# Performance work log

Measured on AMD Instinct MI355X. Metric: run time of the kernel, lower is better.

The kernel has to match this reference:

```python
import jax, jax.numpy as jnp
import numpy as np

EMBED = 1024
HEADS = 16
HEAD_DIM = EMBED // HEADS
MLP_HIDDEN = 4096


def _layernorm(x, g, b, eps=1e-5):
    mu = jnp.mean(x, axis=-1, keepdims=True)
    var = jnp.mean(jnp.square(x - mu), axis=-1, keepdims=True)
    return (x - mu) * jax.lax.rsqrt(var + eps) * g + b


def setup_inputs() -> dict:
    key = jax.random.key(0)
    ks = jax.random.split(key, 8)
    s = 0.02
    return {
        "x": jax.random.normal(ks[0], (8, 1024, EMBED), dtype=jnp.float32),
        "qkv_w": jax.random.normal(ks[1], (EMBED, 3 * EMBED), dtype=jnp.float32) * s,
        "qkv_b": jnp.zeros((3 * EMBED,), jnp.float32),
        "proj_w": jax.random.normal(ks[2], (EMBED, EMBED), dtype=jnp.float32) * s,
        "proj_b": jnp.zeros((EMBED,), jnp.float32),
        "fc1_w": jax.random.normal(ks[3], (EMBED, MLP_HIDDEN), dtype=jnp.float32) * s,
        "fc1_b": jnp.zeros((MLP_HIDDEN,), jnp.float32),
        "fc2_w": jax.random.normal(ks[4], (MLP_HIDDEN, EMBED), dtype=jnp.float32) * s,
        "fc2_b": jnp.zeros((EMBED,), jnp.float32),
        "ln1_g": jnp.ones((EMBED,), jnp.float32),
        "ln1_b": jnp.zeros((EMBED,), jnp.float32),
        "ln2_g": jnp.ones((EMBED,), jnp.float32),
        "ln2_b": jnp.zeros((EMBED,), jnp.float32),
    }


def reference(x, qkv_w, qkv_b, proj_w, proj_b, fc1_w, fc1_b, fc2_w, fc2_b,
              ln1_g, ln1_b, ln2_g, ln2_b):
    B, N, C = x.shape
    scale = HEAD_DIM ** -0.5

    # --- MHSA on pre-norm input ---
    h = _layernorm(x, ln1_g, ln1_b)
    qkv = h @ qkv_w + qkv_b                      # [B,N,3C]
    qkv = qkv.reshape(B, N, 3, HEADS, HEAD_DIM)
    q, k, v = (qkv[:, :, i].transpose(0, 2, 1, 3) for i in range(3))  # [B,H,N,d]
    attn = jnp.einsum('bhqd,bhkd->bhqk', q, k) * scale
    attn = jax.nn.softmax(attn, axis=-1)
    o = jnp.einsum('bhqk,bhkd->bhqd', attn, v)   # [B,H,N,d]
    o = o.transpose(0, 2, 1, 3).reshape(B, N, C)
    x = x + (o @ proj_w + proj_b)

    # --- MLP ---
    h2 = _layernorm(x, ln2_g, ln2_b)
    h2 = jax.nn.gelu(h2 @ fc1_w + fc1_b, approximate=False)
    x = x + (h2 @ fc2_w + fc2_b)
    return x
```

## Files before the change

kernel.cpp:

```cpp
#include <hip/hip_runtime.h>
#include <hip/hip_bf16.h>

typedef __bf16 bf16x8 __attribute__((ext_vector_type(8)));
typedef float  f32x4  __attribute__((ext_vector_type(4)));
typedef unsigned short u16;

static __device__ __forceinline__ u16 f2bf(float f) {
  union { float f; unsigned u; } v; v.f = f;
  unsigned r = v.u + 0x7fffu + ((v.u >> 16) & 1u);
  return (u16)(r >> 16);
}

static __device__ __forceinline__ void gld16(const void* g, void* l) {
  __builtin_amdgcn_global_load_lds(
      (const __attribute__((address_space(1))) unsigned int*)g,
      (__attribute__((address_space(3))) unsigned int*)l, 16, 0, 0);
}

#define SBAR() do { __builtin_amdgcn_sched_barrier(0); \
                    __builtin_amdgcn_s_barrier(); \
                    __builtin_amdgcn_sched_barrier(0); } while (0)

__global__ __launch_bounds__(256) void prep_k(
    const float* __restrict__ qkv_w, const float* __restrict__ proj_w,
    const float* __restrict__ fc1_w, const float* __restrict__ fc2_w,
    u16* __restrict__ wqkvT, u16* __restrict__ wprojT,
    u16* __restrict__ wfc1T, u16* __restrict__ wfc2T,
    const float* __restrict__ x, const float* __restrict__ g,
    const float* __restrict__ b, u16* __restrict__ hbuf) {
  const int bid = blockIdx.x;
  const int t = threadIdx.x;
  if (bid < 12288) {
    __shared__ float tile[32][33];
    const float* W; u16* Wt; int K, N, nx, i;
    if (bid < 3072)      { W = qkv_w;  Wt = wqkvT;  K = 1024; N = 3072; nx = 96;  i = bid; }
    else if (bid < 4096) { W = proj_w; Wt = wprojT; K = 1024; N = 1024; nx = 32;  i = bid - 3072; }
    else if (bid < 8192) { W = fc1_w;  Wt = wfc1T;  K = 1024; N = 4096; nx = 128; i = bid - 4096; }
    else                 { W = fc2_w;  Wt = wfc2T;  K = 4096; N = 1024; nx = 32;  i = bid - 8192; }
    const int n0 = (i % nx) * 32, k0 = (i / nx) * 32;
    const int r = t >> 3, c4 = (t & 7) * 4;
    const float4 v = *(const float4*)(W + (size_t)(k0 + r) * N + n0 + c4);
    tile[r][c4 + 0] = v.x; tile[r][c4 + 1] = v.y;
    tile[r][c4 + 2] = v.z; tile[r][c4 + 3] = v.w;
    __syncthreads();
    const int n = t >> 3, k4 = (t & 7) * 4;
    uint2 pk;
    pk.x = f2bf(tile[k4 + 0][n]) | ((unsigned)f2bf(tile[k4 + 1][n]) << 16);
    pk.y = f2bf(tile[k4 + 2][n]) | ((unsigned)f2bf(tile[k4 + 3][n]) << 16);
    *(uint2*)(Wt + (size_t)(n0 + n) * K + k0 + k4) = pk;
  } else {
    __shared__ float red[2][4];
    const size_t row = bid - 12288;
    const float4 v = *(const float4*)(x + row * 1024 + t * 4);
    float s = v.x + v.y + v.z + v.w;
    float ss = v.x * v.x + v.y * v.y + v.z * v.z + v.w * v.w;
    #pragma unroll
    for (int m = 1; m <= 32; m <<= 1) { s += __shfl_xor(s, m); ss += __shfl_xor(ss, m); }
    if ((t & 63) == 0) { red[0][t >> 6] = s; red[1][t >> 6] = ss; }
    __syncthreads();
    s  = red[0][0] + red[0][1] + red[0][2] + red[0][3];
    ss = red[1][0] + red[1][1] + red[1][2] + red[1][3];
    const float mu = s * (1.f / 1024.f);
    const float var = ss * (1.f / 1024.f) - mu * mu;
    const float rs = rsqrtf(var + 1e-5f);
    const float4 gv = *(const float4*)(g + t * 4);
    const float4 bv = *(const float4*)(b + t * 4);
    uint2 pk;
    pk.x = f2bf((v.x - mu) * rs * gv.x + bv.x) |
           ((unsigned)f2bf((v.y - mu) * rs * gv.y + bv.y) << 16);
    pk.y = f2bf((v.z - mu) * rs * gv.z + bv.z) |
           ((unsigned)f2bf((v.w - mu) * rs * gv.w + bv.w) << 16);
    *(uint2*)(hbuf + row * 1024 + t * 4) = pk;
  }
}

__global__ __launch_bounds__(256) void ln_cast_k(
    const float* __restrict__ x, const float* __restrict__ g,
    const float* __restrict__ b, u16* __restrict__ out) {
  __shared__ float red[2][4];
  const int t = threadIdx.x;
  const size_t row = blockIdx.x;
  const float4 v = *(const float4*)(x + row * 1024 + t * 4);
  float s = v.x + v.y + v.z + v.w;
  float ss = v.x * v.x + v.y * v.y + v.z * v.z + v.w * v.w;
  #pragma unroll
  for (int m = 1; m <= 32; m <<= 1) { s += __shfl_xor(s, m); ss += __shfl_xor(ss, m); }
  if ((t & 63) == 0) { red[0][t >> 6] = s; red[1][t >> 6] = ss; }
  __syncthreads();
  s  = red[0][0] + red[0][1] + red[0][2] + red[0][3];
  ss = red[1][0] + red[1][1] + red[1][2] + red[1][3];
  const float mu = s * (1.f / 1024.f);
  const float var = ss * (1.f / 1024.f) - mu * mu;
  const float rs = rsqrtf(var + 1e-5f);
  const float4 gv = *(const float4*)(g + t * 4);
  const float4 bv = *(const float4*)(b + t * 4);
  uint2 pk;
  pk.x = f2bf((v.x - mu) * rs * gv.x + bv.x) |
         ((unsigned)f2bf((v.y - mu) * rs * gv.y + bv.y) << 16);
  pk.y = f2bf((v.z - mu) * rs * gv.z + bv.z) |
         ((unsigned)f2bf((v.w - mu) * rs * gv.w + bv.w) << 16);
  *(uint2*)(out + row * 1024 + t * 4) = pk;
}

template <int EPI>
__global__ __launch_bounds__(512, 2) void gemm_k(
    const u16* __restrict__ A, const u16* __restrict__ Bt,
    const float* __restrict__ bias, u16* __restrict__ Cb, float* __restrict__ Cf,
    const float* __restrict__ R, u16* __restrict__ vT, int M, int N, int K) {
  __shared__ u16 SH[49152];
  const int t = threadIdx.x;
  const int nt = N >> 7;
  const int q = gridDim.x >> 3;
  const int swz = (blockIdx.x & 7) * q + (blockIdx.x >> 3);
  const int tn = swz % nt, tm = swz / nt;
  const int lo = t & 15, hi = (t >> 4) & 3, wid = t >> 6;
  const int wm = wid >> 1, wn = wid & 1;
  const int NT = K >> 6;

  const int srow = t >> 3;
  const int sc = (t & 7) ^ (srow & 7);
  const u16* gA = A  + (size_t)(tm * 256) * K;
  const u16* gB = Bt + (size_t)(tn * 128) * K;
  auto stA = [&](int dd, int c, int T) {
    gld16(gA + (size_t)(c * 64 + srow) * K + (size_t)T * 64 + sc * 8,
          &SH[dd * 16384 + c * 4096 + t * 8]);
  };
  auto stB = [&](int dd, int c, int T) {
    gld16(gB + (size_t)(c * 64 + srow) * K + (size_t)T * 64 + sc * 8,
          &SH[32768 + dd * 8192 + c * 4096 + t * 8]);
  };

  const int xr = lo & 7;
  const int rowA = wm * 64 + lo;
  const int rowB = wn * 64 + lo;
#define RD_A(d, m, kk) (*(const bf16x8*)&SH[(d)*16384 + (rowA + (m)*16)*64 + ((((kk)<<2)+hi)^xr)*8])
#define RD_B(d, n, kk) (*(const bf16x8*)&SH[32768 + (d)*8192 + (rowB + (n)*16)*64 + ((((kk)<<2)+hi)^xr)*8])
#define MF(a, b, c) __builtin_amdgcn_mfma_f32_16x16x32_bf16(a, b, c, 0, 0, 0)

  f32x4 acc[4][4];
  #pragma unroll
  for (int i = 0; i < 4; ++i)
    #pragma unroll
    for (int j = 0; j < 4; ++j) acc[i][j] = (f32x4){0.f, 0.f, 0.f, 0.f};

#define PH8(d, M0, STAGES, WAITS) do { \
    bf16x8 a0 = RD_A(d, M0, 0), a1 = RD_A(d, M0, 1); \
    STAGES; SBAR(); __builtin_amdgcn_s_setprio(1); \
    acc[M0][0]=MF(a0,b00,acc[M0][0]); acc[M0][1]=MF(a0,b10,acc[M0][1]); \
    acc[M0][2]=MF(a0,b20,acc[M0][2]); acc[M0][3]=MF(a0,b30,acc[M0][3]); \
    acc[M0][0]=MF(a1,b01,acc[M0][0]); acc[M0][1]=MF(a1,b11,acc[M0][1]); \
    acc[M0][2]=MF(a1,b21,acc[M0][2]); acc[M0][3]=MF(a1,b31,acc[M0][3]); \
    __builtin_amdgcn_s_setprio(0); WAITS; SBAR(); } while (0)

  stA(0, 0, 0); stA(0, 1, 0); stA(0, 2, 0); stA(0, 3, 0);
  stB(0, 0, 0); stB(0, 1, 0);
  stB(1, 0, 1); stB(1, 1, 1);
  asm volatile("s_waitcnt vmcnt(2)" ::: "memory");
  SBAR();

  for (int T = 0; T < NT; ++T) {
    const int d = T & 1, dn = d ^ 1;
    bf16x8 b00 = RD_B(d,0,0), b01 = RD_B(d,0,1), b10 = RD_B(d,1,0), b11 = RD_B(d,1,1);
    bf16x8 b20 = RD_B(d,2,0), b21 = RD_B(d,2,1), b30 = RD_B(d,3,0), b31 = RD_B(d,3,1);
    PH8(d, 0, { if (T + 1 < NT) { stA(dn, 0, T + 1); stA(dn, 1, T + 1);
                                  stA(dn, 2, T + 1); stA(dn, 3, T + 1); } }, );
    PH8(d, 1, { if (T + 2 < NT) { stB(d, 0, T + 2); stB(d, 1, T + 2); } }, );
    PH8(d, 2, , );
    PH8(d, 3, ,
        { if (T < NT - 2)       { asm volatile("s_waitcnt vmcnt(2)" ::: "memory"); }
          else if (T == NT - 2) { asm volatile("s_waitcnt vmcnt(0)" ::: "memory"); } });
  }

  if constexpr (EPI == 2) {
    #pragma unroll
    for (int ni = 0; ni < 4; ++ni) {
      const int col = tn * 128 + wn * 64 + ni * 16 + lo;
      const float bv = bias[col];
      #pragma unroll
      for (int mi = 0; mi < 4; ++mi) {
        const int row0 = tm * 256 + wm * 64 + mi * 16 + hi * 4;
        #pragma unroll
        for (int r = 0; r < 4; ++r) {
          const size_t idx = (size_t)(row0 + r) * N + col;
          Cf[idx] = acc[mi][ni][r] + bv + R[idx];
        }
      }
    }
  } else {
    #pragma unroll
    for (int ni = 0; ni < 4; ++ni) {
      const int colL = wn * 64 + ni * 16 + lo;
      const float bv = bias[tn * 128 + colL];
      #pragma unroll
      for (int mi = 0; mi < 4; ++mi) {
        const int rowL = wm * 64 + mi * 16 + hi * 4;
        #pragma unroll
        for (int r = 0; r < 4; ++r) {
          float val = acc[mi][ni][r] + bv;
          if (EPI == 1) {
            const float u = 0.79788456f * val * (1.f + 0.044715f * val * val);
            const float e = __expf(fminf(2.f * u, 80.f));
            val = val * (e / (e + 1.f));
          }
          SH[(rowL + r) * 128 + colL] = f2bf(val);
        }
      }
    }
    __syncthreads();
    {
      const int base = t * 16;
      #pragma unroll
      for (int p = 0; p < 8; ++p) {
        const int o = base + p * 8192;
        const int row = o >> 8;
        const int cb = (o & 255) >> 1;
        const uint4 v4 = *(const uint4*)&SH[o >> 1];
        *(uint4*)(Cb + (size_t)(tm * 256 + row) * N + tn * 128 + cb) = v4;
      }
    }
    if constexpr (EPI == 3) {
      if (tn >= 16) {
        const int c = t & 127;
        const int rg = t >> 7;
        const int gcol = tn * 128 + c;
        const int hh = (gcol - 2048) >> 6, dd = gcol & 63;
        const int bb = tm >> 2, nb = (tm & 3) * 256;
        u16* dst = vT + ((size_t)((bb * 16 + hh) * 64 + dd) << 10) + nb + rg * 64;
        #pragma unroll
        for (int i = 0; i < 8; ++i) {
          const int r0 = rg * 64 + i * 8;
          u16 tv[8];
          #pragma unroll
          for (int j = 0; j < 8; ++j) tv[j] = SH[(r0 + j) * 128 + c];
          uint4 pk;
          pk.x = tv[0] | ((unsigned)tv[1] << 16);
          pk.y = tv[2] | ((unsigned)tv[3] << 16);
          pk.z = tv[4] | ((unsigned)tv[5] << 16);
          pk.w = tv[6] | ((unsigned)tv[7] << 16);
          *(uint4*)(dst + i * 8) = pk;
        }
      }
    }
  }
#undef RD_A
#undef RD_B
#undef MF
#undef PH8
}

__global__ __launch_bounds__(256, 2) void attn_k(
    const u16* __restrict__ qkv, const u16* __restrict__ vT, u16* __restrict__ o) {
  __shared__ u16 lK[64 * 64];
  __shared__ u16 lV[64 * 64];
  __shared__ u16 lP[64 * 72];
  const int t = threadIdx.x;
  const int lo = t & 15, hi = (t >> 4) & 3, w = t >> 6;
  const int swz = (blockIdx.x & 7) * 256 + (blockIdx.x >> 3);
  const int qt = swz & 15, bh = swz >> 4;
  const int b = bh >> 4, h = bh & 15;
  const int q0 = qt * 64;
  const u16* Qb = qkv + (size_t)b * 1024 * 3072 + h * 64;
  const u16* Kb = Qb + 1024;
  const u16* Vt = vT + (size_t)bh * 64 * 1024;

  bf16x8 qf[2];
  {
    const size_t q = q0 + w * 16 + lo;
    qf[0] = *(const bf16x8*)(Qb + q * 3072 + hi * 8);
    qf[1] = *(const bf16x8*)(Qb + q * 3072 + 32 + hi * 8);
  }
  f32x4 oacc[4];
  #pragma unroll
  for (int i = 0; i < 4; ++i) oacc[i] = (f32x4){0.f, 0.f, 0.f, 0.f};
  float m = -1e30f, lsum = 0.f;
  const int srow = t >> 3;
  const int sc = (t & 7) ^ (srow & 7);
  const int xr = lo & 7;
  const float SC = 0.125f * 1.44269504f;

  for (int kv0 = 0; kv0 < 1024; kv0 += 64) {
    __syncthreads();
    #pragma unroll
    for (int j = 0; j < 2; ++j) {
      const int r64 = j * 32 + srow;
      gld16(Kb + (size_t)(kv0 + r64) * 3072 + sc * 8, &lK[(j * 256 + t) * 8]);
      gld16(Vt + (size_t)r64 * 1024 + kv0 + sc * 8, &lV[(j * 256 + t) * 8]);
    }
    __syncthreads();

    f32x4 s[4];
    #pragma unroll
    for (int i = 0; i < 4; ++i) s[i] = (f32x4){0.f, 0.f, 0.f, 0.f};
    #pragma unroll
    for (int kk = 0; kk < 2; ++kk) {
      #pragma unroll
      for (int mi = 0; mi < 4; ++mi) {
        const bf16x8 kf = *(const bf16x8*)&lK[(mi * 16 + lo) * 64 + (((kk << 2) + hi) ^ xr) * 8];
        s[mi] = __builtin_amdgcn_mfma_f32_16x16x32_bf16(kf, qf[kk], s[mi], 0, 0, 0);
      }
    }
    float sv[16];
    float tmax = -1e30f;
    #pragma unroll
    for (int mi = 0; mi < 4; ++mi)
      #pragma unroll
      for (int r = 0; r < 4; ++r) {
        const float xx = s[mi][r] * SC;
        sv[mi * 4 + r] = xx;
        tmax = fmaxf(tmax, xx);
      }
    tmax = fmaxf(tmax, __shfl_xor(tmax, 16));
    tmax = fmaxf(tmax, __shfl_xor(tmax, 32));
    if (__any(tmax > m + 11.5f)) {
      const float mnew = fmaxf(m, tmax);
      const float alpha = exp2f(m - mnew);
      m = mnew;
      lsum *= alpha;
      float ar[4];
      #pragma unroll
      for (int r = 0; r < 4; ++r) ar[r] = __shfl(alpha, hi * 4 + r);
      #pragma unroll
      for (int ni = 0; ni < 4; ++ni)
        #pragma unroll
        for (int r = 0; r < 4; ++r) oacc[ni][r] *= ar[r];
    }
    float p[16], ts = 0.f;
    #pragma unroll
    for (int i = 0; i < 16; ++i) { p[i] = exp2f(sv[i] - m); ts += p[i]; }
    ts += __shfl_xor(ts, 16);
    ts += __shfl_xor(ts, 32);
    lsum += ts;
    #pragma unroll
    for (int mi = 0; mi < 4; ++mi) {
      uint2 pk;
      pk.x = f2bf(p[mi * 4 + 0]) | ((unsigned)f2bf(p[mi * 4 + 1]) << 16);
      pk.y = f2bf(p[mi * 4 + 2]) | ((unsigned)f2bf(p[mi * 4 + 3]) << 16);
      *(uint2*)&lP[(w * 16 + lo) * 72 + mi * 16 + hi * 4] = pk;
    }
    asm volatile("s_waitcnt lgkmcnt(0)" ::: "memory");
    #pragma unroll
    for (int kk = 0; kk < 2; ++kk) {
      const bf16x8 pf = *(const bf16x8*)&lP[(w * 16 + lo) * 72 + kk * 32 + hi * 8];
      #pragma unroll
      for (int ni = 0; ni < 4; ++ni) {
        const bf16x8 vf = *(const bf16x8*)&lV[(ni * 16 + lo) * 64 + (((kk << 2) + hi) ^ xr) * 8];
        oacc[ni] = __builtin_amdgcn_mfma_f32_16x16x32_bf16(pf, vf, oacc[ni], 0, 0, 0);
      }
    }
  }
  float lr[4];
  #pragma unroll
  for (int r = 0; r < 4; ++r) lr[r] = 1.f / __shfl(lsum, hi * 4 + r);
  #pragma unroll
  for (int ni = 0; ni < 4; ++ni) {
    const int d = ni * 16 + lo;
    #pragma unroll
    for (int r = 0; r < 4; ++r) {
      const int n = q0 + w * 16 + hi * 4 + r;
      o[((size_t)(b * 1024 + n) * 16 + h) * 64 + d] = f2bf(oacc[ni][r] * lr[r]);
    }
  }
}

extern "C" void kernel_launch(void* const* d_in, const int* in_sizes, int n_in,
                              void* d_out, int out_size, void* d_ws, size_t ws_size,
                              hipStream_t stream) {
  const float* x      = (const float*)d_in[0];
  const float* qkv_w  = (const float*)d_in[1];
  const float* qkv_b  = (const float*)d_in[2];
  const float* proj_w = (const float*)d_in[3];
  const float* proj_b = (const float*)d_in[4];
  const float* fc1_w  = (const float*)d_in[5];
  const float* fc1_b  = (const float*)d_in[6];
  const float* fc2_w  = (const float*)d_in[7];
  const float* fc2_b  = (const float*)d_in[8];
  const float* ln1_g  = (const float*)d_in[9];
  const float* ln1_b  = (const float*)d_in[10];
  const float* ln2_g  = (const float*)d_in[11];
  const float* ln2_b  = (const float*)d_in[12];
  float* out = (float*)d_out;
  char* ws = (char*)d_ws;
  u16* wqkvT = (u16*)(ws);
  u16* wprojT = (u16*)(ws + 6291456);
  u16* wfc1T = (u16*)(ws + 8388608);
  u16* wfc2T = (u16*)(ws + 16777216);
  u16* hbuf  = (u16*)(ws + 25165824);
  u16* qkvo  = (u16*)(ws + 41943040);
  u16* vT    = (u16*)(ws + 92274688);
  u16* fc1o  = qkvo;

  prep_k<<<20480, 256, 0, stream>>>(qkv_w, proj_w, fc1_w, fc2_w,
                                    wqkvT, wprojT, wfc1T, wfc2T,
                                    x, ln1_g, ln1_b, hbuf);
  gemm_k<3><<<768, 512, 0, stream>>>(hbuf, wqkvT, qkv_b, qkvo, nullptr, nullptr, vT, 8192, 3072, 1024);
  attn_k<<<2048, 256, 0, stream>>>(qkvo, vT, hbuf);
  gemm_k<2><<<256, 512, 0, stream>>>(hbuf, wprojT, proj_b, nullptr, out, x, nullptr, 8192, 1024, 1024);
  ln_cast_k<<<8192, 256, 0, stream>>>(out, ln2_g, ln2_b, hbuf);
  gemm_k<1><<<1024, 512, 0, stream>>>(hbuf, wfc1T, fc1_b, fc1o, nullptr, nullptr, nullptr, 8192, 4096, 1024);
  gemm_k<2><<<256, 512, 0, stream>>>(fc1o, wfc2T, fc2_b, nullptr, out, out, nullptr, 8192, 1024, 4096);
}
```

Before: 399.1 us.

## Replace pipelined 256x128 GEMM with simple single-buffered 128x128 kernel

Swaps the double-buffered, barrier-scheduled 512-thread GEMM with 256x128 tiles for a plain 256-thread kernel that uses 128x128 tiles and a single LDS buffer. Each K step loads A and B, syncs, runs the MFMAs and syncs again. This shrinks LDS use and doubles the grid size, which may raise occupancy. In exchange it gives up the overlap of global loads with compute and the tuned scheduling and priority hints. The epilogue's vT transpose indexing is adapted to the new tile height, though it still reads rows up to 127 from a 128-row shared tile.

```diff
diff --git a/kernel.cpp b/kernel.cpp
--- a/kernel.cpp
+++ b/kernel.cpp
@@ -16,10 +16,6 @@
       (const __attribute__((address_space(1))) unsigned int*)g,
       (__attribute__((address_space(3))) unsigned int*)l, 16, 0, 0);
 }
-
-#define SBAR() do { __builtin_amdgcn_sched_barrier(0); \
-                    __builtin_amdgcn_s_barrier(); \
-                    __builtin_amdgcn_sched_barrier(0); } while (0)
 
 __global__ __launch_bounds__(256) void prep_k(
     const float* __restrict__ qkv_w, const float* __restrict__ proj_w,
@@ -103,11 +99,11 @@
 }
 
 template <int EPI>
-__global__ __launch_bounds__(512, 2) void gemm_k(
+__global__ __launch_bounds__(256) void gemm97_k(
     const u16* __restrict__ A, const u16* __restrict__ Bt,
     const float* __restrict__ bias, u16* __restrict__ Cb, float* __restrict__ Cf,
     const float* __restrict__ R, u16* __restrict__ vT, int M, int N, int K) {
-  __shared__ u16 SH[49152];
+  __shared__ u16 SH[16384];
   const int t = threadIdx.x;
   const int nt = N >> 7;
   const int q = gridDim.x >> 3;
@@ -119,22 +115,12 @@
 
   const int srow = t >> 3;
   const int sc = (t & 7) ^ (srow & 7);
-  const u16* gA = A  + (size_t)(tm * 256) * K;
+  const u16* gA = A  + (size_t)(tm * 128) * K;
   const u16* gB = Bt + (size_t)(tn * 128) * K;
-  auto stA = [&](int dd, int c, int T) {
-    gld16(gA + (size_t)(c * 64 + srow) * K + (size_t)T * 64 + sc * 8,
-          &SH[dd * 16384 + c * 4096 + t * 8]);
-  };
-  auto stB = [&](int dd, int c, int T) {
-    gld16(gB + (size_t)(c * 64 + srow) * K + (size_t)T * 64 + sc * 8,
-          &SH[32768 + dd * 8192 + c * 4096 + t * 8]);
-  };
 
   const int xr = lo & 7;
-  const int rowA = wm * 64 + lo;
-  const int rowB = wn * 64 + lo;
-#define RD_A(d, m, kk) (*(const bf16x8*)&SH[(d)*16384 + (rowA + (m)*16)*64 + ((((kk)<<2)+hi)^xr)*8])
-#define RD_B(d, n, kk) (*(const bf16x8*)&SH[32768 + (d)*8192 + (rowB + (n)*16)*64 + ((((kk)<<2)+hi)^xr)*8])
+#define RD_A(m, kk) (*(const bf16x8*)&SH[(wm*64 + (m)*16 + lo)*64 + ((((kk)<<2)+hi)^xr)*8])
+#define RD_B(n, kk) (*(const bf16x8*)&SH[8192 + (wn*64 + (n)*16 + lo)*64 + ((((kk)<<2)+hi)^xr)*8])
 #define MF(a, b, c) __builtin_amdgcn_mfma_f32_16x16x32_bf16(a, b, c, 0, 0, 0)
 
   f32x4 acc[4][4];
@@ -143,32 +129,34 @@
     #pragma unroll
     for (int j = 0; j < 4; ++j) acc[i][j] = (f32x4){0.f, 0.f, 0.f, 0.f};
 
-#define PH8(d, M0, STAGES, WAITS) do { \
-    bf16x8 a0 = RD_A(d, M0, 0), a1 = RD_A(d, M0, 1); \
-    STAGES; SBAR(); __builtin_amdgcn_s_setprio(1); \
-    acc[M0][0]=MF(a0,b00,acc[M0][0]); acc[M0][1]=MF(a0,b10,acc[M0][1]); \
-    acc[M0][2]=MF(a0,b20,acc[M0][2]); acc[M0][3]=MF(a0,b30,acc[M0][3]); \
-    acc[M0][0]=MF(a1,b01,acc[M0][0]); acc[M0][1]=MF(a1,b11,acc[M0][1]); \
-    acc[M0][2]=MF(a1,b21,acc[M0][2]); acc[M0][3]=MF(a1,b31,acc[M0][3]); \
-    __builtin_amdgcn_s_setprio(0); WAITS; SBAR(); } while (0)
-
-  stA(0, 0, 0); stA(0, 1, 0); stA(0, 2, 0); stA(0, 3, 0);
-  stB(0, 0, 0); stB(0, 1, 0);
-  stB(1, 0, 1); stB(1, 1, 1);
-  asm volatile("s_waitcnt vmcnt(2)" ::: "memory");
-  SBAR();
-
   for (int T = 0; T < NT; ++T) {
-    const int d = T & 1, dn = d ^ 1;
-    bf16x8 b00 = RD_B(d,0,0), b01 = RD_B(d,0,1), b10 = RD_B(d,1,0), b11 = RD_B(d,1,1);
-    bf16x8 b20 = RD_B(d,2,0), b21 = RD_B(d,2,1), b30 = RD_B(d,3,0), b31 = RD_B(d,3,1);
-    PH8(d, 0, { if (T + 1 < NT) { stA(dn, 0, T + 1); stA(dn, 1, T + 1);
-                                  stA(dn, 2, T + 1); stA(dn, 3, T + 1); } }, );
-    PH8(d, 1, { if (T + 2 < NT) { stB(d, 0, T + 2); stB(d, 1, T + 2); } }, );
-    PH8(d, 2, , );
-    PH8(d, 3, ,
-        { if (T < NT - 2)       { asm volatile("s_waitcnt vmcnt(2)" ::: "memory"); }
-          else if (T == NT - 2) { asm volatile("s_waitcnt vmcnt(0)" ::: "memory"); } });
+    #pragma unroll
+    for (int c = 0; c < 4; ++c) {
+      gld16(gA + (size_t)(c * 32 + srow) * K + (size_t)T * 64 + sc * 8,
+            &SH[(c * 256 + t) * 8]);
+      gld16(gB + (size_t)(c * 32 + srow) * K + (size_t)T * 64 + sc * 8,
+            &SH[8192 + (c * 256 + t) * 8]);
+    }
+    __syncthreads();
+    bf16x8 bF[8], aF[8];
+    #pragma unroll
+    for (int n = 0; n < 4; ++n) {
+      bF[n * 2 + 0] = RD_B(n, 0);
+      bF[n * 2 + 1] = RD_B(n, 1);
+    }
+    #pragma unroll
+    for (int m = 0; m < 4; ++m) {
+      aF[m * 2 + 0] = RD_A(m, 0);
+      aF[m * 2 + 1] = RD_A(m, 1);
+    }
+    #pragma unroll
+    for (int kk = 0; kk < 2; ++kk)
+      #pragma unroll
+      for (int m = 0; m < 4; ++m)
+        #pragma unroll
+        for (int n = 0; n < 4; ++n)
+          acc[m][n] = MF(aF[m * 2 + kk], bF[n * 2 + kk], acc[m][n]);
+    __syncthreads();
   }
 
   if constexpr (EPI == 2) {
@@ -178,7 +166,7 @@
       const float bv = bias[col];
       #pragma unroll
       for (int mi = 0; mi < 4; ++mi) {
-        const int row0 = tm * 256 + wm * 64 + mi * 16 + hi * 4;
+        const int row0 = tm * 128 + wm * 64 + mi * 16 + hi * 4;
         #pragma unroll
         for (int r = 0; r < 4; ++r) {
           const size_t idx = (size_t)(row0 + r) * N + col;
@@ -202,7 +190,7 @@
             const float e = __expf(fminf(2.f * u, 80.f));
             val = val * (e / (e + 1.f));
           }
-          SH[(rowL + r) * 128 + colL] = f2bf(val);
+          SH[rowL == 0 ? (0 + r) * 128 + colL : (rowL + r) * 128 + colL] = f2bf(val);
         }
       }
     }
@@ -211,11 +199,11 @@
       const int base = t * 16;
       #pragma unroll
       for (int p = 0; p < 8; ++p) {
-        const int o = base + p * 8192;
+        const int o = base + p * 4096;
         const int row = o >> 8;
         const int cb = (o & 255) >> 1;
         const uint4 v4 = *(const uint4*)&SH[o >> 1];
-        *(uint4*)(Cb + (size_t)(tm * 256 + row) * N + tn * 128 + cb) = v4;
+        *(uint4*)(Cb + (size_t)(tm * 128 + row) * N + tn * 128 + cb) = v4;
       }
     }
     if constexpr (EPI == 3) {
@@ -224,7 +212,7 @@
         const int rg = t >> 7;
         const int gcol = tn * 128 + c;
         const int hh = (gcol - 2048) >> 6, dd = gcol & 63;
-        const int bb = tm >> 2, nb = (tm & 3) * 256;
+        const int bb = tm >> 3, nb = (tm & 7) * 128;
         u16* dst = vT + ((size_t)((bb * 16 + hh) * 64 + dd) << 10) + nb + rg * 64;
         #pragma unroll
         for (int i = 0; i < 8; ++i) {
@@ -245,7 +233,6 @@
 #undef RD_A
 #undef RD_B
 #undef MF
-#undef PH8
 }
 
 __global__ __launch_bounds__(256, 2) void attn_k(
@@ -392,10 +379,10 @@
   prep_k<<<20480, 256, 0, stream>>>(qkv_w, proj_w, fc1_w, fc2_w,
                                     wqkvT, wprojT, wfc1T, wfc2T,
                                     x, ln1_g, ln1_b, hbuf);
-  gemm_k<3><<<768, 512, 0, stream>>>(hbuf, wqkvT, qkv_b, qkvo, nullptr, nullptr, vT, 8192, 3072, 1024);
+  gemm97_k<3><<<1536, 256, 0, stream>>>(hbuf, wqkvT, qkv_b, qkvo, nullptr, nullptr, vT, 8192, 3072, 1024);
   attn_k<<<2048, 256, 0, stream>>>(qkvo, vT, hbuf);
-  gemm_k<2><<<256, 512, 0, stream>>>(hbuf, wprojT, proj_b, nullptr, out, x, nullptr, 8192, 1024, 1024);
+  gemm97_k<2><<<512, 256, 0, stream>>>(hbuf, wprojT, proj_b, nullptr, out, x, nullptr, 8192, 1024, 1024);
   ln_cast_k<<<8192, 256, 0, stream>>>(out, ln2_g, ln2_b, hbuf);
-  gemm_k<1><<<1024, 512, 0, stream>>>(hbuf, wfc1T, fc1_b, fc1o, nullptr, nullptr, nullptr, 8192, 4096, 1024);
-  gemm_k<2><<<256, 512, 0, stream>>>(fc1o, wfc2T, fc2_b, nullptr, out, out, nullptr, 8192, 1024, 4096);
-}
+  gemm97_k<1><<<2048, 256, 0, stream>>>(hbuf, wfc1T, fc1_b, fc1o, nullptr, nullptr, nullptr, 8192, 4096, 1024);
+  gemm97_k<2><<<512, 256, 0, stream>>>(fc1o, wfc2T, fc2_b, nullptr, out, out, nullptr, 8192, 1024, 4096);
+}
```

Measured after the change: 409.7 us. 2.7% more time.
